# Performance work log

Measured on AMD Instinct MI355X. Metric: run time of the kernel, lower is better.

## Reference

```python
import jax, jax.numpy as jnp
import numpy as np

EMBED_DIM = 256
NUM_HEADS = 8
HEAD_DIM = EMBED_DIM // NUM_HEADS


def setup_inputs() -> dict:
    key0 = jax.random.key(0)
    ks = jax.random.split(key0, 12)
    B, T, S, E = 4, 256, 16384, EMBED_DIM
    inv = 1.0 / np.sqrt(E)
    inputs = {
        "query": jax.random.normal(ks[0], (B, T, E), dtype=jnp.float32),
        "key": jax.random.normal(ks[1], (B, S, E), dtype=jnp.float32),
        "value": jax.random.normal(ks[2], (B, S, E), dtype=jnp.float32),
        "mask": jax.random.uniform(ks[3], (B, T, S), dtype=jnp.float32),
        # nn.MultiheadAttention in-projection (split into q/k/v parts) and out-projection
        "Wq": jax.random.uniform(ks[4], (E, E), jnp.float32, -inv, inv),
        "bq": jnp.zeros((E,), jnp.float32),
        "Wk": jax.random.uniform(ks[5], (E, E), jnp.float32, -inv, inv),
        "bk": jnp.zeros((E,), jnp.float32),
        "Wv": jax.random.uniform(ks[6], (E, E), jnp.float32, -inv, inv),
        "bv": jnp.zeros((E,), jnp.float32),
        "Wo": jax.random.uniform(ks[7], (E, E), jnp.float32, -inv, inv),
        "bo": jnp.zeros((E,), jnp.float32),
        # fixed default scaling factors (num_heads must be 8)
        "scaling_factors": jnp.asarray([32.0, 32.0, 16.0, 16.0, 8.0, 8.0, 4.0, 4.0], jnp.float32),
    }
    return inputs


def reference(query, key, value, mask, Wq, bq, Wk, bk, Wv, bv, Wo, bo, scaling_factors):
    B, T, E = query.shape
    S = key.shape[1]
    H, D = NUM_HEADS, HEAD_DIM
    # input projections (torch Linear convention: x @ W.T + b)
    q = (query @ Wq.T + bq).reshape(B, T, H, D).transpose(0, 2, 1, 3)  # [B,H,T,D]
    k = (key @ Wk.T + bk).reshape(B, S, H, D).transpose(0, 2, 1, 3)    # [B,H,S,D]
    v = (value @ Wv.T + bv).reshape(B, S, H, D).transpose(0, 2, 1, 3)  # [B,H,S,D]
    scale = 1.0 / jnp.sqrt(jnp.asarray(D, query.dtype))
    scores = jnp.einsum("bhtd,bhsd->bhts", q * scale, k)               # [B,H,T,S]
    # per-head scaled soft mask added as attention bias
    bias = mask[:, None, :, :] * scaling_factors[None, :, None, None]  # [B,H,T,S]
    attn = jax.nn.softmax(scores + bias, axis=-1)
    out = jnp.einsum("bhts,bhsd->bhtd", attn, v)                       # [B,H,T,D]
    out = out.transpose(0, 2, 1, 3).reshape(B, T, E)
    return out @ Wo.T + bo
```

## Files before the change

### kernel.cpp

```cpp
#include <hip/hip_runtime.h>

#define B_ 4
#define T_ 256
#define S_ 16384
#define E_ 256
#define H_ 8
#define D_ 32

typedef _Float16 f16;
typedef _Float16 f16x2 __attribute__((ext_vector_type(2)));
typedef _Float16 f16x4 __attribute__((ext_vector_type(4)));
typedef _Float16 f16x8 __attribute__((ext_vector_type(8)));
typedef float f32x4 __attribute__((ext_vector_type(4)));

typedef const __attribute__((address_space(1))) void* gas_t;
typedef __attribute__((address_space(3))) void* las_t;

__device__ __forceinline__ void gload_lds16(const void* g, void* l) {
    __builtin_amdgcn_global_load_lds((gas_t)g, (las_t)l, 16, 0, 0);
}

__device__ __forceinline__ f16x2 cvt_pk_f16(float a, float b) {
    return __builtin_bit_cast(f16x2, __builtin_amdgcn_cvt_pkrtz(a, b));
}

__device__ __forceinline__ f16x8 pack8(float4 a, float4 b) {
    f16x2 p0 = cvt_pk_f16(a.x, a.y), p1 = cvt_pk_f16(a.z, a.w);
    f16x2 p2 = cvt_pk_f16(b.x, b.y), p3 = cvt_pk_f16(b.z, b.w);
    return (f16x8){p0[0], p0[1], p1[0], p1[1], p2[0], p2[1], p3[0], p3[1]};
}

#define LOG2E 1.4426950408889634f

template <int MODE>
__device__ __forceinline__ void proj2_body(
    char* lbase, const float* __restrict__ in, const float* __restrict__ W,
    const float* __restrict__ bias, f16* __restrict__ out, int row0, float oscale)
{
    constexpr int NT = 8;
    int tid = threadIdx.x;
    int wv = tid >> 6, ln = tid & 63, g = ln >> 4, lc = ln & 15;

    f16x8 wf[2][8];
    #pragma unroll
    for (int ni = 0; ni < 2; ni++) {
        const float* wp = W + (size_t)(wv * 32 + ni * 16 + lc) * 256 + g * 8;
        #pragma unroll
        for (int ks = 0; ks < 8; ks++) {
            float4 a = *(const float4*)(wp + ks * 32);
            float4 b = *(const float4*)(wp + ks * 32 + 4);
            wf[ni][ks] = pack8(a, b);
        }
    }
    float bl[2][4], bn[2];
    if (MODE == 1) {
        #pragma unroll
        for (int ni = 0; ni < 2; ni++) bn[ni] = bias[wv * 32 + ni * 16 + lc];
    } else {
        #pragma unroll
        for (int ni = 0; ni < 2; ni++)
            #pragma unroll
            for (int r = 0; r < 4; r++) bl[ni][r] = bias[wv * 32 + ni * 16 + g * 4 + r];
    }

    int srow = tid >> 5, sc = tid & 31;
    int scs = (sc & 24) | ((sc ^ srow) & 7);
    const float* gsrc = in + (size_t)(row0 + srow) * 256 + sc * 8;
    int ldoff = srow * 512 + scs * 16;
    int bb = row0 >> 14, sbase = row0 & 16383;

    float4 r0[NT], r1[NT];
    auto issue = [&](int t) {
        const float* p = gsrc + (size_t)t * 4096;
        r0[t] = *(const float4*)p;
        r1[t] = *(const float4*)(p + 4);
    };
    auto wr = [&](int t) {
        *(f16x8*)(lbase + (t % 3) * 8192 + ldoff) = pack8(r0[t], r1[t]);
    };

    issue(0); issue(1);
    asm volatile("s_waitcnt vmcnt(2)" ::: "memory");
    wr(0);
    issue(2);
    asm volatile("s_waitcnt vmcnt(2)" ::: "memory");
    wr(1);
    asm volatile("s_waitcnt lgkmcnt(0)" ::: "memory");
    __builtin_amdgcn_s_barrier();

    #pragma unroll
    for (int t = 0; t < NT; t++) {
        f32x4 a0 = {0.f, 0.f, 0.f, 0.f}, a1 = {0.f, 0.f, 0.f, 0.f};
        #pragma unroll
        for (int ks = 0; ks < 8; ks++) {
            int c = ks * 4 + g;
            int cs = (c & 24) | ((c ^ lc) & 7);
            f16x8 af = *(const f16x8*)(lbase + (t % 3) * 8192 + lc * 512 + cs * 16);
            if (MODE == 1) {
                a0 = __builtin_amdgcn_mfma_f32_16x16x32_f16(af, wf[0][ks], a0, 0, 0, 0);
                a1 = __builtin_amdgcn_mfma_f32_16x16x32_f16(af, wf[1][ks], a1, 0, 0, 0);
            } else {
                a0 = __builtin_amdgcn_mfma_f32_16x16x32_f16(wf[0][ks], af, a0, 0, 0, 0);
                a1 = __builtin_amdgcn_mfma_f32_16x16x32_f16(wf[1][ks], af, a1, 0, 0, 0);
            }
        }
        if (MODE == 1) {
            f16x4 h0, h1;
            #pragma unroll
            for (int r = 0; r < 4; r++) {
                h0[r] = (f16)(a0[r] + bn[0]);
                h1[r] = (f16)(a1[r] + bn[1]);
            }
            int s = sbase + t * 16 + g * 4;
            *(f16x4*)(out + ((size_t)(bb * 256 + wv * 32 + lc) << 14) + s) = h0;
            *(f16x4*)(out + ((size_t)(bb * 256 + wv * 32 + 16 + lc) << 14) + s) = h1;
        } else {
            f16x4 h0, h1;
            #pragma unroll
            for (int r = 0; r < 4; r++) {
                h0[r] = (f16)((a0[r] + bl[0][r]) * oscale);
                h1[r] = (f16)((a1[r] + bl[1][r]) * oscale);
            }
            size_t rowb = (size_t)(row0 + t * 16 + lc) * 256;
            *(f16x4*)(out + rowb + wv * 32 + g * 4) = h0;
            *(f16x4*)(out + rowb + wv * 32 + 16 + g * 4) = h1;
        }
        if (t + 3 < NT) issue(t + 3);
        if (t + 2 < NT) {
            if (t + 3 < NT) { asm volatile("s_waitcnt vmcnt(4)" ::: "memory"); }
            else            { asm volatile("s_waitcnt vmcnt(2)" ::: "memory"); }
            wr(t + 2);
            asm volatile("s_waitcnt lgkmcnt(0)" ::: "memory");
            __builtin_amdgcn_s_barrier();
        }
    }
}

__global__ __launch_bounds__(512, 4) void proj_fused2(
    const float* __restrict__ query, const float* __restrict__ key, const float* __restrict__ value,
    const float* __restrict__ Wq, const float* __restrict__ Wk, const float* __restrict__ Wv,
    const float* __restrict__ bq, const float* __restrict__ bk, const float* __restrict__ bv,
    f16* __restrict__ q16, f16* __restrict__ k16, f16* __restrict__ v16T, float qscale)
{
    __shared__ __align__(16) f16 AT[3][4096];
    char* lb = (char*)&AT[0][0];
    int bx = blockIdx.x;
    if (bx < 512)       proj2_body<0>(lb, key,   Wk, bk, k16,  bx * 128, 1.0f);
    else if (bx < 1024) proj2_body<1>(lb, value, Wv, bv, v16T, (bx - 512) * 128, 1.0f);
    else                proj2_body<2>(lb, query, Wq, bq, q16,  (bx - 1024) * 128, qscale);
}

__global__ __launch_bounds__(256, 4) void out_proj(
    const float* __restrict__ in, const float* __restrict__ w,
    const float* __restrict__ bias, float* __restrict__ outp)
{
    __shared__ __align__(16) f16 SMEM[16896];
    f16 (*As)[264] = (f16(*)[264])SMEM;
    f16 (*Bs)[264] = (f16(*)[264])(SMEM + 32 * 264);
    int bid = blockIdx.x + blockIdx.y * 32;
    int tid = threadIdx.x;
    int wq = tid >> 6, ln = tid & 63, g = ln >> 4, lc = ln & 15;
    int row0 = (bid & 31) * 32;
    int n0 = (bid >> 5) * 32;
    {
        int r = tid >> 3, q0 = (tid & 7) * 32;
        const float* ip = in + (size_t)(row0 + r) * 256 + q0;
        #pragma unroll
        for (int i = 0; i < 4; i++) {
            float4 v0 = *(const float4*)(ip + i * 8);
            float4 v1 = *(const float4*)(ip + i * 8 + 4);
            *(f16x8*)&As[r][q0 + i * 8] = pack8(v0, v1);
        }
        const float* wp = w + (size_t)(n0 + r) * 256 + q0;
        #pragma unroll
        for (int i = 0; i < 4; i++) {
            float4 v0 = *(const float4*)(wp + i * 8);
            float4 v1 = *(const float4*)(wp + i * 8 + 4);
            *(f16x8*)&Bs[r][q0 + i * 8] = pack8(v0, v1);
        }
    }
    __syncthreads();
    int mi = wq >> 1, ni = wq & 1;
    f32x4 acc = {0.f, 0.f, 0.f, 0.f};
    #pragma unroll
    for (int ks = 0; ks < 8; ks++) {
        f16x8 a = *(const f16x8*)&As[mi * 16 + lc][ks * 32 + g * 8];
        f16x8 bf = *(const f16x8*)&Bs[ni * 16 + lc][ks * 32 + g * 8];
        acc = __builtin_amdgcn_mfma_f32_16x16x32_f16(a, bf, acc, 0, 0, 0);
    }
    int n = n0 + ni * 16 + lc;
    float bv = bias[n];
    #pragma unroll
    for (int r = 0; r < 4; r++) {
        int row = row0 + mi * 16 + g * 4 + r;
        outp[(size_t)row * 256 + n] = acc[r] + bv;
    }
}

__global__ __launch_bounds__(1024, 4) void attn_kernel(
    const f16* __restrict__ q16,
    const f16* __restrict__ k16,
    const f16* __restrict__ v16T,
    const float* __restrict__ mask,
    const float* __restrict__ scal,
    float* __restrict__ partO, float* __restrict__ partL)
{
    constexpr int ITERS = 16;
    __shared__ __align__(16) f16 KT[3][32 * 256];
    __shared__ __align__(16) f16 VT[3][256 * 32];
    __shared__ __align__(16) float MT[3][128 * 32];

    int raw = blockIdx.x;
    int th = raw >> 7, b = (raw >> 5) & 3, ck = raw & 31;
    int tid = threadIdx.x;
    int wv = tid >> 6;
    int h = wv & 7, tsub = wv >> 3;
    int ln = tid & 63, g = ln >> 4, lc = ln & 15;
    int t0 = th * 128, s0 = ck * 512;

    float sc_h = scal[h] * LOG2E;
    float negfix = -(sc_h + 4.0f);

    f16x8 qf[4];
    #pragma unroll
    for (int tl = 0; tl < 4; tl++) {
        const f16* qp = q16 + (size_t)(b * T_ + t0 + tsub * 64 + tl * 16 + lc) * E_ + h * 32 + g * 8;
        qf[tl] = *(const f16x8*)qp;
    }

    f32x4 oac[4][2];
    float l_part[4];
    #pragma unroll
    for (int tl = 0; tl < 4; tl++) {
        oac[tl][0] = (f32x4){0.f, 0.f, 0.f, 0.f};
        oac[tl][1] = (f32x4){0.f, 0.f, 0.f, 0.f};
        l_part[tl] = 0.f;
    }

    auto stage = [&](int it, int bufi) {
        int sg0 = s0 + it * 32;
        {
            int sl = wv * 2 + (ln >> 5);
            int slot = (sl ^ (sl >> 3)) & 7;
            int jc = (ln & 31) ^ slot;
            gload_lds16(k16 + (size_t)(b * S_ + sg0 + sl) * E_ + jc * 8,
                        (char*)&KT[bufi][0] + wv * 1024);
        }
        {
            int dl = wv * 16 + (ln >> 2);
            int srcj = (ln & 3) ^ ((dl >> 1) & 3);
            gload_lds16(v16T + (size_t)(b * E_ + dl) * S_ + sg0 + srcj * 8,
                        (char*)&VT[bufi][0] + wv * 1024);
        }
        {
            int r = ln >> 3;
            int sj = (ln & 7) ^ r;
            gload_lds16(mask + (size_t)(b * T_ + t0 + wv * 8 + r) * S_ + sg0 + sj * 4,
                        (char*)&MT[bufi][0] + wv * 1024);
        }
    };

    stage(0, 0);
    stage(1, 1);

    f32x4 zero4 = {0.f, 0.f, 0.f, 0.f};
    int ib = 0;

    #pragma unroll 1
    for (int it = 0; it < ITERS; it++) {
        if (it + 1 < ITERS) { asm volatile("s_waitcnt vmcnt(3)" ::: "memory"); }
        else                { asm volatile("s_waitcnt vmcnt(0)" ::: "memory"); }
        __builtin_amdgcn_s_barrier();
        asm volatile("" ::: "memory");
        if (it + 2 < ITERS) {
            int wb = ib + 2; if (wb >= 3) wb -= 3;
            stage(it + 2, wb);
        }

        f16x8 kb[2];
        #pragma unroll
        for (int si = 0; si < 2; si++) {
            int sl = si * 16 + lc;
            int slot = (sl ^ (sl >> 3)) & 7;
            int j = (h * 4 + g) ^ slot;
            kb[si] = *(const f16x8*)((char*)&KT[ib][0] + sl * 512 + j * 16);
        }
        f16x4 va[2][2];
        #pragma unroll
        for (int si = 0; si < 2; si++) {
            #pragma unroll
            for (int ni = 0; ni < 2; ni++) {
                int d = h * 32 + ni * 16 + lc;
                int u = (si * 2 + (g >> 1)) ^ ((d >> 1) & 3);
                va[si][ni] = *(const f16x4*)((char*)&VT[ib][0] + d * 64 + u * 16 + (g & 1) * 8);
            }
        }

        #pragma unroll
        for (int tl = 0; tl < 4; tl++) {
            int t = tsub * 64 + tl * 16 + lc;
            const float4 mf0 = *(const float4*)((char*)&MT[ib][0] + t * 128 + (((g    ) ^ (t & 7)) << 4));
            const float4 mf1 = *(const float4*)((char*)&MT[ib][0] + t * 128 + (((4 + g) ^ (t & 7)) << 4));
            f32x4 st0 = __builtin_amdgcn_mfma_f32_16x16x32_f16(kb[0], qf[tl], zero4, 0, 0, 0);
            f32x4 st1 = __builtin_amdgcn_mfma_f32_16x16x32_f16(kb[1], qf[tl], zero4, 0, 0, 0);
            float p0 = __builtin_amdgcn_exp2f(st0[0] + __builtin_fmaf(mf0.x, sc_h, negfix));
            float p1 = __builtin_amdgcn_exp2f(st0[1] + __builtin_fmaf(mf0.y, sc_h, negfix));
            float p2 = __builtin_amdgcn_exp2f(st0[2] + __builtin_fmaf(mf0.z, sc_h, negfix));
            float p3 = __builtin_amdgcn_exp2f(st0[3] + __builtin_fmaf(mf0.w, sc_h, negfix));
            float p4 = __builtin_amdgcn_exp2f(st1[0] + __builtin_fmaf(mf1.x, sc_h, negfix));
            float p5 = __builtin_amdgcn_exp2f(st1[1] + __builtin_fmaf(mf1.y, sc_h, negfix));
            float p6 = __builtin_amdgcn_exp2f(st1[2] + __builtin_fmaf(mf1.z, sc_h, negfix));
            float p7 = __builtin_amdgcn_exp2f(st1[3] + __builtin_fmaf(mf1.w, sc_h, negfix));
            l_part[tl] += ((p0 + p1) + (p2 + p3)) + ((p4 + p5) + (p6 + p7));
            f16x2 c01 = cvt_pk_f16(p0, p1);
            f16x2 c23 = cvt_pk_f16(p2, p3);
            f16x2 c45 = cvt_pk_f16(p4, p5);
            f16x2 c67 = cvt_pk_f16(p6, p7);
            f16x4 pb0 = {c01[0], c01[1], c23[0], c23[1]};
            f16x4 pb1 = {c45[0], c45[1], c67[0], c67[1]};
            oac[tl][0] = __builtin_amdgcn_mfma_f32_16x16x16f16(va[0][0], pb0, oac[tl][0], 0, 0, 0);
            oac[tl][0] = __builtin_amdgcn_mfma_f32_16x16x16f16(va[1][0], pb1, oac[tl][0], 0, 0, 0);
            oac[tl][1] = __builtin_amdgcn_mfma_f32_16x16x16f16(va[0][1], pb0, oac[tl][1], 0, 0, 0);
            oac[tl][1] = __builtin_amdgcn_mfma_f32_16x16x16f16(va[1][1], pb1, oac[tl][1], 0, 0, 0);
        }
        ib++; if (ib >= 3) ib -= 3;
    }

    #pragma unroll
    for (int tl = 0; tl < 4; tl++) {
        float lv = l_part[tl];
        lv += __shfl_xor(lv, 16, 64);
        lv += __shfl_xor(lv, 32, 64);
        l_part[tl] = lv;
    }
    float* po = partO + (size_t)raw * 128 * 256;
    #pragma unroll
    for (int tl = 0; tl < 4; tl++) {
        #pragma unroll
        for (int ni = 0; ni < 2; ni++) {
            float4 o4 = {oac[tl][ni][0], oac[tl][ni][1], oac[tl][ni][2], oac[tl][ni][3]};
            *(float4*)(po + (size_t)(tsub * 64 + tl * 16 + lc) * 256 + h * 32 + ni * 16 + g * 4) = o4;
        }
    }
    if (g == 0) {
        float* pl = partL + (size_t)raw * 128 * 8;
        #pragma unroll
        for (int tl = 0; tl < 4; tl++) {
            int trow = tsub * 64 + tl * 16 + lc;
            pl[trow * 8 + h] = l_part[tl];
        }
    }
}

__global__ __launch_bounds__(256) void combine_kernel(
    const float* __restrict__ partO, const float* __restrict__ partL,
    float* __restrict__ attnO)
{
    int bid = blockIdx.x;
    int b = bid >> 8, t = bid & 255;
    int th = t >> 7, tl = t & 127;
    int tid = threadIdx.x;
    __shared__ float sl[32][8];
    {
        int ck = tid >> 3, hh = tid & 7;
        size_t blk = (size_t)(th * 128 + b * 32 + ck);
        sl[ck][hh] = partL[blk * 1024 + tl * 8 + hh];
    }
    __syncthreads();
    int h = tid >> 5;
    float L = 0.f;
    #pragma unroll 8
    for (int ck = 0; ck < 32; ck++) L += sl[ck][h];
    float acc = 0.f;
    #pragma unroll 4
    for (int ck = 0; ck < 32; ck++) {
        size_t blk = (size_t)(th * 128 + b * 32 + ck);
        acc += partO[blk * 32768 + (size_t)tl * 256 + tid];
    }
    attnO[(size_t)bid * 256 + tid] = acc / L;
}

extern "C" void kernel_launch(void* const* d_in, const int* in_sizes, int n_in,
                              void* d_out, int out_size, void* d_ws, size_t ws_size,
                              hipStream_t stream) {
    (void)in_sizes; (void)n_in; (void)out_size; (void)ws_size;
    const float* query = (const float*)d_in[0];
    const float* key   = (const float*)d_in[1];
    const float* value = (const float*)d_in[2];
    const float* mask  = (const float*)d_in[3];
    const float* Wq = (const float*)d_in[4];
    const float* bq = (const float*)d_in[5];
    const float* Wk = (const float*)d_in[6];
    const float* bk = (const float*)d_in[7];
    const float* Wv = (const float*)d_in[8];
    const float* bv = (const float*)d_in[9];
    const float* Wo = (const float*)d_in[10];
    const float* bo = (const float*)d_in[11];
    const float* scal = (const float*)d_in[12];

    char* ws = (char*)d_ws;
    f16* q16  = (f16*)(ws + (4 << 17));
    float* attnO = (float*)(ws + 1048576);
    f16* k16  = (f16*)(ws + 2097152);
    f16* v16T = (f16*)(ws + 35651584);
    float* partO = (float*)(ws + 69206016);
    float* partL = (float*)(ws + 103809024);

    const float qscale = 0.17677669529663687f * LOG2E;
    proj_fused2<<<1032, 512, 0, stream>>>(query, key, value, Wq, Wk, Wv,
                                          bq, bk, bv, q16, k16, v16T, qscale);

    attn_kernel<<<256, 1024, 0, stream>>>(q16, k16, v16T, mask, scal, partO, partL);
    combine_kernel<<<1024, 256, 0, stream>>>(partO, partL, attnO);

    out_proj<<<dim3(32, 8), 256, 0, stream>>>(attnO, Wo, bo, (float*)d_out);
}
```

Before: 147.9 us.

## Restructure projection kernel to 1024 threads with one 16-column tile per wave

The fused Q/K/V projection kernel now launches 1024 threads per block, with 16 waves each owning a 16-wide output slice instead of 8 waves owning 32. Each thread loads one float4 per tile, and the LDS layout switches from an XOR swizzle to padded rows. Weight loads are split in two halves overlapped with the first input tile loads, and output stores are buffered and written at the end. The aim is more memory-level parallelism and lower register pressure per thread for this bandwidth-bound stage, at the cost of smaller per-wave MFMA work and delayed stores.

```diff
diff --git a/kernel.cpp b/kernel.cpp
--- a/kernel.cpp
+++ b/kernel.cpp
@@ -33,121 +33,111 @@
 #define LOG2E 1.4426950408889634f
 
 template <int MODE>
-__device__ __forceinline__ void proj2_body(
+__device__ __forceinline__ void proj3_body(
     char* lbase, const float* __restrict__ in, const float* __restrict__ W,
     const float* __restrict__ bias, f16* __restrict__ out, int row0, float oscale)
 {
     constexpr int NT = 8;
+    constexpr int TS = 8448;
     int tid = threadIdx.x;
-    int wv = tid >> 6, ln = tid & 63, g = ln >> 4, lc = ln & 15;
-
-    f16x8 wf[2][8];
-    #pragma unroll
-    for (int ni = 0; ni < 2; ni++) {
-        const float* wp = W + (size_t)(wv * 32 + ni * 16 + lc) * 256 + g * 8;
-        #pragma unroll
-        for (int ks = 0; ks < 8; ks++) {
-            float4 a = *(const float4*)(wp + ks * 32);
-            float4 b = *(const float4*)(wp + ks * 32 + 4);
-            wf[ni][ks] = pack8(a, b);
-        }
-    }
-    float bl[2][4], bn[2];
-    if (MODE == 1) {
-        #pragma unroll
-        for (int ni = 0; ni < 2; ni++) bn[ni] = bias[wv * 32 + ni * 16 + lc];
-    } else {
-        #pragma unroll
-        for (int ni = 0; ni < 2; ni++)
-            #pragma unroll
-            for (int r = 0; r < 4; r++) bl[ni][r] = bias[wv * 32 + ni * 16 + g * 4 + r];
-    }
-
-    int srow = tid >> 5, sc = tid & 31;
-    int scs = (sc & 24) | ((sc ^ srow) & 7);
-    const float* gsrc = in + (size_t)(row0 + srow) * 256 + sc * 8;
-    int ldoff = srow * 512 + scs * 16;
-    int bb = row0 >> 14, sbase = row0 & 16383;
-
-    float4 r0[NT], r1[NT];
-    auto issue = [&](int t) {
-        const float* p = gsrc + (size_t)t * 4096;
-        r0[t] = *(const float4*)p;
-        r1[t] = *(const float4*)(p + 4);
+    int wq = tid >> 6, ln = tid & 63, g = ln >> 4, lc = ln & 15;
+
+    const float* gsrc = in + (size_t)(row0 + wq) * 256 + ln * 4;
+    int ldwr = wq * 528 + ln * 8;
+
+    float4 Lr[NT];
+    auto issue = [&](int t) { Lr[t] = *(const float4*)(gsrc + (size_t)t * 4096); };
+    auto wr = [&](int t) {
+        float4 v = Lr[t];
+        f16x4 h = {(f16)v.x, (f16)v.y, (f16)v.z, (f16)v.w};
+        *(f16x4*)(lbase + (t % 3) * TS + ldwr) = h;
     };
-    auto wr = [&](int t) {
-        *(f16x8*)(lbase + (t % 3) * 8192 + ldoff) = pack8(r0[t], r1[t]);
-    };
-
-    issue(0); issue(1);
-    asm volatile("s_waitcnt vmcnt(2)" ::: "memory");
-    wr(0);
-    issue(2);
-    asm volatile("s_waitcnt vmcnt(2)" ::: "memory");
-    wr(1);
+
+    issue(0); issue(1); issue(2);
+    const float* wp = W + (size_t)(wq * 16 + lc) * 256 + g * 8;
+    f16x8 wf[8];
+    {
+        float4 wt[8];
+        #pragma unroll
+        for (int ks = 0; ks < 4; ks++) {
+            wt[2 * ks]     = *(const float4*)(wp + ks * 32);
+            wt[2 * ks + 1] = *(const float4*)(wp + ks * 32 + 4);
+        }
+        asm volatile("s_waitcnt vmcnt(0)" ::: "memory");
+        wr(0); wr(1);
+        #pragma unroll
+        for (int ks = 0; ks < 4; ks++) wf[ks] = pack8(wt[2 * ks], wt[2 * ks + 1]);
+        #pragma unroll
+        for (int ks = 4; ks < 8; ks++) {
+            wt[2 * (ks - 4)]     = *(const float4*)(wp + ks * 32);
+            wt[2 * (ks - 4) + 1] = *(const float4*)(wp + ks * 32 + 4);
+        }
+        asm volatile("s_waitcnt vmcnt(0)" ::: "memory");
+        #pragma unroll
+        for (int ks = 4; ks < 8; ks++) wf[ks] = pack8(wt[2 * (ks - 4)], wt[2 * (ks - 4) + 1]);
+    }
     asm volatile("s_waitcnt lgkmcnt(0)" ::: "memory");
     __builtin_amdgcn_s_barrier();
 
+    float bl[4], bn;
+    if (MODE == 1) {
+        bn = bias[wq * 16 + lc];
+    } else {
+        #pragma unroll
+        for (int r = 0; r < 4; r++) bl[r] = bias[wq * 16 + g * 4 + r];
+    }
+
+    f16x4 hbuf[NT];
+    f32x4 zero4 = {0.f, 0.f, 0.f, 0.f};
+
     #pragma unroll
     for (int t = 0; t < NT; t++) {
-        f32x4 a0 = {0.f, 0.f, 0.f, 0.f}, a1 = {0.f, 0.f, 0.f, 0.f};
+        f32x4 acc = zero4;
         #pragma unroll
         for (int ks = 0; ks < 8; ks++) {
-            int c = ks * 4 + g;
-            int cs = (c & 24) | ((c ^ lc) & 7);
-            f16x8 af = *(const f16x8*)(lbase + (t % 3) * 8192 + lc * 512 + cs * 16);
-            if (MODE == 1) {
-                a0 = __builtin_amdgcn_mfma_f32_16x16x32_f16(af, wf[0][ks], a0, 0, 0, 0);
-                a1 = __builtin_amdgcn_mfma_f32_16x16x32_f16(af, wf[1][ks], a1, 0, 0, 0);
-            } else {
-                a0 = __builtin_amdgcn_mfma_f32_16x16x32_f16(wf[0][ks], af, a0, 0, 0, 0);
-                a1 = __builtin_amdgcn_mfma_f32_16x16x32_f16(wf[1][ks], af, a1, 0, 0, 0);
-            }
+            f16x8 af = *(const f16x8*)(lbase + (t % 3) * TS + lc * 528 + (ks * 4 + g) * 16);
+            if (MODE == 1) acc = __builtin_amdgcn_mfma_f32_16x16x32_f16(af, wf[ks], acc, 0, 0, 0);
+            else           acc = __builtin_amdgcn_mfma_f32_16x16x32_f16(wf[ks], af, acc, 0, 0, 0);
         }
         if (MODE == 1) {
-            f16x4 h0, h1;
             #pragma unroll
-            for (int r = 0; r < 4; r++) {
-                h0[r] = (f16)(a0[r] + bn[0]);
-                h1[r] = (f16)(a1[r] + bn[1]);
-            }
-            int s = sbase + t * 16 + g * 4;
-            *(f16x4*)(out + ((size_t)(bb * 256 + wv * 32 + lc) << 14) + s) = h0;
-            *(f16x4*)(out + ((size_t)(bb * 256 + wv * 32 + 16 + lc) << 14) + s) = h1;
+            for (int r = 0; r < 4; r++) hbuf[t][r] = (f16)(acc[r] + bn);
         } else {
-            f16x4 h0, h1;
             #pragma unroll
-            for (int r = 0; r < 4; r++) {
-                h0[r] = (f16)((a0[r] + bl[0][r]) * oscale);
-                h1[r] = (f16)((a1[r] + bl[1][r]) * oscale);
-            }
-            size_t rowb = (size_t)(row0 + t * 16 + lc) * 256;
-            *(f16x4*)(out + rowb + wv * 32 + g * 4) = h0;
-            *(f16x4*)(out + rowb + wv * 32 + 16 + g * 4) = h1;
+            for (int r = 0; r < 4; r++) hbuf[t][r] = (f16)((acc[r] + bl[r]) * oscale);
         }
         if (t + 3 < NT) issue(t + 3);
         if (t + 2 < NT) {
-            if (t + 3 < NT) { asm volatile("s_waitcnt vmcnt(4)" ::: "memory"); }
-            else            { asm volatile("s_waitcnt vmcnt(2)" ::: "memory"); }
+            if (t + 3 < NT) { asm volatile("s_waitcnt vmcnt(1)" ::: "memory"); }
+            else            { asm volatile("s_waitcnt vmcnt(0)" ::: "memory"); }
             wr(t + 2);
             asm volatile("s_waitcnt lgkmcnt(0)" ::: "memory");
             __builtin_amdgcn_s_barrier();
         }
     }
-}
-
-__global__ __launch_bounds__(512, 4) void proj_fused2(
+
+    if (MODE == 1) {
+        f16* ob = out + (((size_t)((row0 >> 14) * 256 + wq * 16 + lc)) << 14) + (row0 & 16383) + g * 4;
+        #pragma unroll
+        for (int t = 0; t < NT; t++) *(f16x4*)(ob + t * 16) = hbuf[t];
+    } else {
+        f16* ob = out + (size_t)(row0 + lc) * 256 + wq * 16 + g * 4;
+        #pragma unroll
+        for (int t = 0; t < NT; t++) *(f16x4*)(ob + (size_t)t * 16 * 256) = hbuf[t];
+    }
+}
+
+__global__ __launch_bounds__(1024, 4) void proj_fused3(
     const float* __restrict__ query, const float* __restrict__ key, const float* __restrict__ value,
     const float* __restrict__ Wq, const float* __restrict__ Wk, const float* __restrict__ Wv,
     const float* __restrict__ bq, const float* __restrict__ bk, const float* __restrict__ bv,
     f16* __restrict__ q16, f16* __restrict__ k16, f16* __restrict__ v16T, float qscale)
 {
-    __shared__ __align__(16) f16 AT[3][4096];
-    char* lb = (char*)&AT[0][0];
+    __shared__ __align__(16) char LB[3 * 8448];
     int bx = blockIdx.x;
-    if (bx < 512)       proj2_body<0>(lb, key,   Wk, bk, k16,  bx * 128, 1.0f);
-    else if (bx < 1024) proj2_body<1>(lb, value, Wv, bv, v16T, (bx - 512) * 128, 1.0f);
-    else                proj2_body<2>(lb, query, Wq, bq, q16,  (bx - 1024) * 128, qscale);
+    if (bx < 512)       proj3_body<0>(LB, key,   Wk, bk, k16,  bx * 128, 1.0f);
+    else if (bx < 1024) proj3_body<1>(LB, value, Wv, bv, v16T, (bx - 512) * 128, 1.0f);
+    else                proj3_body<2>(LB, query, Wq, bq, q16,  (bx - 1024) * 128, qscale);
 }
 
 __global__ __launch_bounds__(256, 4) void out_proj(
@@ -407,8 +397,8 @@
     float* partL = (float*)(ws + 103809024);
 
     const float qscale = 0.17677669529663687f * LOG2E;
-    proj_fused2<<<1032, 512, 0, stream>>>(query, key, value, Wq, Wk, Wv,
-                                          bq, bk, bv, q16, k16, v16T, qscale);
+    proj_fused3<<<1032, 1024, 0, stream>>>(query, key, value, Wq, Wk, Wv,
+                                           bq, bk, bv, q16, k16, v16T, qscale);
 
     attn_kernel<<<256, 1024, 0, stream>>>(q16, k16, v16T, mask, scal, partO, partL);
     combine_kernel<<<1024, 256, 0, stream>>>(partO, partL, attnO);
```

After: 170.8 us. 1.15x slower.
